# Kernel tuning notes

Measured on AMD Instinct MI355X. Metric: run time of the kernel, lower is better.

The kernel has to match this reference:

```python
import jax, jax.numpy as jnp
import numpy as np

B, S, J, D, H = 8, 256, 24, 128, 8
DEPTH = D // H  # 16


def _pos_encoding(seq_len, d_model):
    # matches position_encoding: angle = pos / 10000^(2*(i//2)/d_model);
    # even dims -> sin, odd dims -> cos. shape (1, seq_len, 1, d_model)
    pos = jnp.arange(seq_len, dtype=jnp.float32)[:, None]
    i = jnp.arange(d_model)
    rates = 1.0 / jnp.power(10000.0, (2 * (i // 2)).astype(jnp.float32) / d_model)
    ang = pos * rates[None, :]
    pe = jnp.where(i % 2 == 0, jnp.sin(ang), jnp.cos(ang))
    return pe[None, :, None, :]


def setup_inputs() -> dict:
    key = jax.random.key(0)
    ks = jax.random.split(key, 10)
    std = float(np.sqrt(1.0 / np.sqrt(D * D)))  # matches initialize()
    x = jax.random.normal(ks[0], (B, S, J, D), jnp.float32)
    # look-ahead mask on the (S-1, S-1) sub-block: 1 = masked (future)
    mask = jnp.triu(jnp.ones((S - 1, S - 1), jnp.float32), k=1)
    Wq = jax.random.normal(ks[1], (D, D), jnp.float32) * std
    bq = jnp.zeros((D,), jnp.float32)
    Wk = jax.random.normal(ks[2], (D, D), jnp.float32) * std
    bk = jnp.zeros((D,), jnp.float32)
    Wv = jax.random.normal(ks[3], (D, D), jnp.float32) * std
    bv = jnp.zeros((D,), jnp.float32)
    Wo = jax.random.normal(ks[4], (D, D), jnp.float32) * std
    bo = jnp.zeros((D,), jnp.float32)
    return {"x": x, "mask": mask, "Wq": Wq, "bq": bq, "Wk": Wk, "bk": bk,
            "Wv": Wv, "bv": bv, "Wo": Wo, "bo": bo}


def _split_heads(t):
    # (B, S, J, D) -> (B, J, H, S, DEPTH)
    b, s, j, d = t.shape
    t = t.transpose(0, 2, 1, 3)                 # (B, J, S, D)
    t = t.reshape(b, j, s, H, DEPTH)            # (B, J, S, H, DEPTH)
    return t.transpose(0, 1, 3, 2, 4)           # (B, J, H, S, DEPTH)


def reference(x, mask, Wq, bq, Wk, bk, Wv, bv, Wo, bo):
    b, s, j, d = x.shape
    x = x + _pos_encoding(S, D)[:, :s]          # broadcast over batch & joints
    # shared QKV projections (same math as linear applied on (J,B,S,D))
    q = _split_heads(jnp.einsum('bsjd,de->bsje', x, Wq) + bq)
    k = _split_heads(jnp.einsum('bsjd,de->bsje', x, Wk) + bk)
    v = _split_heads(jnp.einsum('bsjd,de->bsje', x, Wv) + bv)
    scores = jnp.einsum('bjhqd,bjhkd->bjhqk', q, k) / jnp.sqrt(
        jnp.asarray(DEPTH, x.dtype))            # (B, J, H, S, S)
    # custom partial-block masking: only the [1:, 1:] sub-block is masked
    scores = scores.at[:, :, :, 1:, 1:].add(mask * -1e9)
    w = jax.nn.softmax(scores, axis=-1)
    out = jnp.einsum('bjhqk,bjhkd->bjhqd', w, v)  # (B, J, H, S, DEPTH)
    out = out.transpose(0, 3, 1, 2, 4).reshape(b, s, j, d)
    out = jnp.einsum('bsjd,de->bsje', out, Wo) + bo
    return (out, mask)
```

## Files before the change

kernel.cpp:

```cpp
#include <hip/hip_runtime.h>
#include <hip/hip_bf16.h>
#include <math.h>

#define NB 8
#define NS 256
#define NJ 24
#define ND 128
#define NH 8
#define NDEP 16
#define NROW (NB * NS * NJ)

typedef unsigned short u16;
typedef unsigned int u32;
typedef float f32x4 __attribute__((ext_vector_type(4)));
typedef short bf16x8 __attribute__((ext_vector_type(8)));
typedef unsigned short us8 __attribute__((ext_vector_type(8)));
typedef unsigned short us4 __attribute__((ext_vector_type(4)));

#define MFMA16(a, b, c) __builtin_amdgcn_mfma_f32_16x16x32_bf16(a, b, c, 0, 0, 0)

#define QSCALE 0.36067376022224085f

__device__ __forceinline__ u16 f2bf(float f) {
    union { __hip_bfloat16 h; u16 u; } cv;
    cv.h = __float2bfloat16(f);
    return cv.u;
}
__device__ __forceinline__ u32 cvtpk(float lo, float hi) {
    u32 r;
    asm("v_cvt_pk_bf16_f32 %0, %1, %2" : "=v"(r) : "v"(lo), "v"(hi));
    return r;
}

__global__ __launch_bounds__(256) void prep_kernel(
        const float* __restrict__ Wq, const float* __restrict__ Wk,
        const float* __restrict__ Wv, const float* __restrict__ Wo,
        const float* __restrict__ mask,
        float* __restrict__ pe, u16* __restrict__ wt,
        float* __restrict__ mask_dst) {
    int idx = blockIdx.x * 256 + threadIdx.x;
    if (idx < 32768) {
        int s = idx >> 7, d = idx & 127;
        float r = __expf(-(float)(d & ~1) * (9.210340371976184f / 128.0f));
        float ang = (float)s * r;
        pe[idx] = (d & 1) ? cosf(ang) : sinf(ang);
    } else if (idx < 98304) {
        int e = idx - 32768;
        int w = e >> 14, rr = e & 16383;
        int n = rr >> 7, kk = rr & 127;
        const float* W = (w == 0) ? Wq : (w == 1) ? Wk : (w == 2) ? Wv : Wo;
        float val = W[kk * 128 + n];
        if (w == 0) val *= QSCALE;
        wt[e] = f2bf(val);
    } else {
        int e = idx - 98304;
        if (e < (NS - 1) * (NS - 1)) mask_dst[e] = mask[e];
    }
}

__global__ __launch_bounds__(256) void qkv_kernel(
        const float* __restrict__ x, const float* __restrict__ pe,
        const u16* __restrict__ wt,
        const float* __restrict__ bq, const float* __restrict__ bk,
        const float* __restrict__ bv,
        u16* __restrict__ qo, u16* __restrict__ ko, u16* __restrict__ vo) {
    __shared__ u16 xs[64][136];
    __shared__ u16 wsh[128][136];
    const int t = threadIdx.x;
    const int row0 = blockIdx.x * 64;

#pragma unroll
    for (int i = 0; i < 8; i++) {
        int f4 = t + i * 256;
        int r = f4 >> 5, c4 = (f4 & 31) * 4;
        int grow = row0 + r;
        int s = (grow / NJ) & (NS - 1);
        float4 xv = *(const float4*)&x[(size_t)grow * ND + c4];
        float4 pv = *(const float4*)&pe[s * ND + c4];
        us4 b4;
        b4[0] = f2bf(xv.x + pv.x); b4[1] = f2bf(xv.y + pv.y);
        b4[2] = f2bf(xv.z + pv.z); b4[3] = f2bf(xv.w + pv.w);
        *(us4*)&xs[r][c4] = b4;
    }

    const int l = t & 63, wv = t >> 6, gg = l >> 4, c = l & 15;
    const float* bm[3] = {bq, bk, bv};
    u16* om[3] = {qo, ko, vo};

#pragma unroll
    for (int w = 0; w < 3; w++) {
        __syncthreads();
#pragma unroll
        for (int i = 0; i < 8; i++) {
            int u8 = t + i * 256;
            int r = u8 >> 4, c8 = (u8 & 15) * 8;
            *(us8*)&wsh[r][c8] = *(const us8*)&wt[w * 16384 + r * 128 + c8];
        }
        __syncthreads();
        f32x4 acc[8] = {};
#pragma unroll
        for (int ks = 0; ks < 4; ks++) {
            bf16x8 af = *(const bf16x8*)&xs[wv * 16 + c][ks * 32 + gg * 8];
#pragma unroll
            for (int nf = 0; nf < 8; nf++) {
                bf16x8 bf_ = *(const bf16x8*)&wsh[nf * 16 + c][ks * 32 + gg * 8];
                acc[nf] = MFMA16(af, bf_, acc[nf]);
            }
        }
        __syncthreads();
        const float bscale = (w == 0) ? QSCALE : 1.0f;
#pragma unroll
        for (int nf = 0; nf < 8; nf++) {
            float bb = bm[w][nf * 16 + c] * bscale;
#pragma unroll
            for (int r = 0; r < 4; r++)
                wsh[wv * 16 + gg * 4 + r][nf * 16 + c] = f2bf(acc[nf][r] + bb);
        }
        __syncthreads();
#pragma unroll
        for (int i = 0; i < 4; i++) {
            int u8 = t + i * 256;
            int row = u8 >> 4, piece = u8 & 15;
            int grow = row0 + row;
            int b = grow / 6144, rem = grow % 6144;
            int s = rem / NJ, jj = rem % NJ;
            int hh = piece >> 1, half = piece & 1;
            us8 val = *(const us8*)&wsh[row][piece * 8];
            *(us8*)&om[w][(size_t)((b * NJ + jj) * NH + hh) * 4096 + s * 16 +
                          half * 8] = val;
        }
    }
}

__global__ __launch_bounds__(512) void attn_kernel(
        const u16* __restrict__ q, const u16* __restrict__ k,
        const u16* __restrict__ v, u16* __restrict__ o) {
    __shared__ u16 ksh[256][24];
    __shared__ uint4 vts4[16][32];

    const int t = threadIdx.x;
    const int bjh = blockIdx.x;
    const size_t base = (size_t)bjh * 4096;

    {
        int row = t >> 1, c8 = (t & 1) * 8;
        *(us8*)&ksh[row][c8] = *(const us8*)&k[base + row * 16 + c8];
    }
    {
        int r = t >> 1, h8 = (t & 1) * 8;
        us8 vv = *(const us8*)&v[base + r * 16 + h8];
        int slot = (r & 0xE0) | ((r & 12) << 1) | ((r & 16) >> 2) | (r & 3);
        int cell = slot >> 3, e = slot & 7;
#pragma unroll
        for (int dd = 0; dd < 8; dd++) {
            int d = h8 + dd;
            ((u16*)&vts4[d][cell ^ (d & 7)])[e] = vv[dd];
        }
    }
    __syncthreads();

    const int wv = t >> 6, l = t & 63, gg = l >> 4, c = l & 15;
    const int h = bjh & 7, j = (bjh >> 3) % NJ, b = bjh / (NJ * NH);
    const size_t obase = (size_t)b * 786432 + (size_t)j * 128 + h * 16 + c;
    const unsigned long long TBL = 0xBA79685F4E3D2C10ull;

#pragma unroll
    for (int slot = 0; slot < 2; slot++) {
        const int g = (int)((TBL >> ((wv * 2 + slot) * 4)) & 15);
        const int dchk = g >> 2;
        const int nch = (g == 0) ? 4 : dchk + 1;
        const int qrow = 16 * g + c;
        const int thr = (qrow == 0) ? 0x7fffffff : qrow;

        bf16x8 bq_ = {};
        if (gg < 2)
            bq_ = *(const bf16x8*)&q[base + (size_t)qrow * 16 + gg * 8];

        f32x4 oa = {};
        float ls = 0.0f;
#pragma unroll
        for (int ch = 0; ch < 4; ch++) {
            if (ch >= nch) continue;
            const bool diag = (g == 0) || (ch == dchk);
            f32x4 st[4];
            __builtin_amdgcn_s_setprio(1);
#pragma unroll
            for (int kf = 0; kf < 4; kf++) {
                bf16x8 ak = {};
                if (gg < 2)
                    ak = *(const bf16x8*)&ksh[ch * 64 + kf * 16 + c][gg * 8];
                f32x4 zz = {};
                st[kf] = MFMA16(ak, bq_, zz);
            }
            __builtin_amdgcn_s_setprio(0);
            u32 pw[8];
            if (diag) {
#pragma unroll
                for (int kf = 0; kf < 4; kf++) {
#pragma unroll
                    for (int r = 0; r < 4; r++) {
                        int key = ch * 64 + kf * 16 + gg * 4 + r;
                        float vv = (key > thr) ? -1.0e9f : st[kf][r];
                        float p = __builtin_amdgcn_exp2f(vv);
                        st[kf][r] = p;
                        ls += p;
                    }
                    pw[kf * 2]     = cvtpk(st[kf][0], st[kf][1]);
                    pw[kf * 2 + 1] = cvtpk(st[kf][2], st[kf][3]);
                }
            } else {
#pragma unroll
                for (int kf = 0; kf < 4; kf++) {
#pragma unroll
                    for (int r = 0; r < 4; r++) {
                        float p = __builtin_amdgcn_exp2f(st[kf][r]);
                        st[kf][r] = p;
                        ls += p;
                    }
                    pw[kf * 2]     = cvtpk(st[kf][0], st[kf][1]);
                    pw[kf * 2 + 1] = cvtpk(st[kf][2], st[kf][3]);
                }
            }
            uint4 a0 = make_uint4(pw[0], pw[1], pw[2], pw[3]);
            uint4 a1 = make_uint4(pw[4], pw[5], pw[6], pw[7]);
            __builtin_amdgcn_s_setprio(1);
#pragma unroll
            for (int ks = 0; ks < 2; ks++) {
                bf16x8 ap = __builtin_bit_cast(bf16x8, ks ? a1 : a0);
                uint4 vb4 = vts4[c][(ch * 8 + ks * 4 + gg) ^ (c & 7)];
                bf16x8 bv_ = __builtin_bit_cast(bf16x8, vb4);
                oa = MFMA16(ap, bv_, oa);
            }
            __builtin_amdgcn_s_setprio(0);
        }
        ls += __shfl_xor(ls, 16);
        ls += __shfl_xor(ls, 32);
        const float inv = 1.0f / ls;
#pragma unroll
        for (int r = 0; r < 4; r++) {
            float ir = __shfl(inv, gg * 4 + r);
            int s = 16 * g + gg * 4 + r;
            o[obase + (size_t)s * 3072] = f2bf(oa[r] * ir);
        }
    }
}

__global__ __launch_bounds__(256) void proj_kernel(
        const u16* __restrict__ in, const u16* __restrict__ wt,
        const float* __restrict__ bias, float* __restrict__ out) {
    __shared__ u16 xs[64][136];
    __shared__ u16 wsh[128][136];
    const int t = threadIdx.x;
    const int row0 = blockIdx.x * 64;
#pragma unroll
    for (int i = 0; i < 4; i++) {
        int u8 = t + i * 256;
        int r = u8 >> 4, c8 = (u8 & 15) * 8;
        *(us8*)&xs[r][c8] = *(const us8*)&in[(size_t)(row0 + r) * ND + c8];
    }
#pragma unroll
    for (int i = 0; i < 8; i++) {
        int u8 = t + i * 256;
        int r = u8 >> 4, c8 = (u8 & 15) * 8;
        *(us8*)&wsh[r][c8] = *(const us8*)&wt[r * 128 + c8];
    }
    __syncthreads();
    const int l = t & 63, wv = t >> 6, gg = l >> 4, c = l & 15;
    f32x4 acc[8] = {};
#pragma unroll
    for (int ks = 0; ks < 4; ks++) {
        bf16x8 af = *(const bf16x8*)&xs[wv * 16 + c][ks * 32 + gg * 8];
#pragma unroll
        for (int nf = 0; nf < 8; nf++) {
            bf16x8 bf_ = *(const bf16x8*)&wsh[nf * 16 + c][ks * 32 + gg * 8];
            acc[nf] = MFMA16(af, bf_, acc[nf]);
        }
    }
    __syncthreads();
    float* bounce = (float*)&wsh[0][0];
#pragma unroll
    for (int nf = 0; nf < 8; nf++) {
        float bb = bias[nf * 16 + c];
#pragma unroll
        for (int r = 0; r < 4; r++)
            bounce[(wv * 16 + gg * 4 + r) * 132 + nf * 16 + c] = acc[nf][r] + bb;
    }
    __syncthreads();
#pragma unroll
    for (int i = 0; i < 8; i++) {
        int idx = t + i * 256;
        int row = idx >> 5, p4 = idx & 31;
        float4 vv = *(const float4*)&bounce[row * 132 + p4 * 4];
        *(float4*)&out[(size_t)(row0 + row) * 128 + p4 * 4] = vv;
    }
}

extern "C" void kernel_launch(void* const* d_in, const int* in_sizes, int n_in,
                              void* d_out, int out_size, void* d_ws, size_t ws_size,
                              hipStream_t stream) {
    const float* x    = (const float*)d_in[0];
    const float* mask = (const float*)d_in[1];
    const float* Wq   = (const float*)d_in[2];
    const float* bq   = (const float*)d_in[3];
    const float* Wk   = (const float*)d_in[4];
    const float* bk   = (const float*)d_in[5];
    const float* Wv   = (const float*)d_in[6];
    const float* bv   = (const float*)d_in[7];
    const float* Wo   = (const float*)d_in[8];
    const float* bo   = (const float*)d_in[9];
    float* out = (float*)d_out;

    char* ws = (char*)d_ws;
    float* pe = (float*)ws;
    u16* wt  = (u16*)(ws + 131072);
    u16* qb  = (u16*)(ws + 262144);
    u16* kb  = qb + (size_t)NROW * ND;
    u16* vb  = kb + (size_t)NROW * ND;
    u16* ab  = vb + (size_t)NROW * ND;

    prep_kernel<<<639, 256, 0, stream>>>(Wq, Wk, Wv, Wo, mask, pe, wt,
                                         out + (size_t)NROW * ND);
    qkv_kernel<<<NROW / 64, 256, 0, stream>>>(x, pe, wt, bq, bk, bv, qb, kb, vb);
    attn_kernel<<<NB * NJ * NH, 512, 0, stream>>>(qb, kb, vb, ab);
    proj_kernel<<<NROW / 64, 256, 0, stream>>>(ab, wt + 3 * 16384, bo, out);
}
```

Before: 57.53 us.

## Read weight fragments directly from global and coalesce attention output writes

The QKV and output-projection kernels stop staging the 128x128 bf16 weight tile in shared memory and load MFMA B fragments straight from global (cache-resident) memory, which shrinks LDS use and removes barriers. The attention kernel now writes its output in the contiguous per-head layout (base + s*16 + c) instead of strided 2-byte scatters, and the projection kernel gathers rows from that head-major layout when loading its A tile. Together these aim to fix uncoalesced stores and to raise occupancy, at the cost of repeated global/L2 weight reads per wave and a gather on the projection input.

```diff
diff --git a/kernel.cpp b/kernel.cpp
--- a/kernel.cpp
+++ b/kernel.cpp
@@ -65,7 +65,7 @@
         const float* __restrict__ bv,
         u16* __restrict__ qo, u16* __restrict__ ko, u16* __restrict__ vo) {
     __shared__ u16 xs[64][136];
-    __shared__ u16 wsh[128][136];
+    __shared__ u16 bounce[64][136];
     const int t = threadIdx.x;
     const int row0 = blockIdx.x * 64;
 
@@ -82,6 +82,7 @@
         b4[2] = f2bf(xv.z + pv.z); b4[3] = f2bf(xv.w + pv.w);
         *(us4*)&xs[r][c4] = b4;
     }
+    __syncthreads();
 
     const int l = t & 63, wv = t >> 6, gg = l >> 4, c = l & 15;
     const float* bm[3] = {bq, bk, bv};
@@ -89,32 +90,25 @@
 
 #pragma unroll
     for (int w = 0; w < 3; w++) {
-        __syncthreads();
-#pragma unroll
-        for (int i = 0; i < 8; i++) {
-            int u8 = t + i * 256;
-            int r = u8 >> 4, c8 = (u8 & 15) * 8;
-            *(us8*)&wsh[r][c8] = *(const us8*)&wt[w * 16384 + r * 128 + c8];
-        }
-        __syncthreads();
         f32x4 acc[8] = {};
 #pragma unroll
         for (int ks = 0; ks < 4; ks++) {
             bf16x8 af = *(const bf16x8*)&xs[wv * 16 + c][ks * 32 + gg * 8];
 #pragma unroll
             for (int nf = 0; nf < 8; nf++) {
-                bf16x8 bf_ = *(const bf16x8*)&wsh[nf * 16 + c][ks * 32 + gg * 8];
+                bf16x8 bf_ = *(const bf16x8*)&wt[w * 16384 + (nf * 16 + c) * 128 +
+                                                 ks * 32 + gg * 8];
                 acc[nf] = MFMA16(af, bf_, acc[nf]);
             }
         }
-        __syncthreads();
+        if (w > 0) __syncthreads();
         const float bscale = (w == 0) ? QSCALE : 1.0f;
 #pragma unroll
         for (int nf = 0; nf < 8; nf++) {
             float bb = bm[w][nf * 16 + c] * bscale;
 #pragma unroll
             for (int r = 0; r < 4; r++)
-                wsh[wv * 16 + gg * 4 + r][nf * 16 + c] = f2bf(acc[nf][r] + bb);
+                bounce[wv * 16 + gg * 4 + r][nf * 16 + c] = f2bf(acc[nf][r] + bb);
         }
         __syncthreads();
 #pragma unroll
@@ -125,7 +119,7 @@
             int b = grow / 6144, rem = grow % 6144;
             int s = rem / NJ, jj = rem % NJ;
             int hh = piece >> 1, half = piece & 1;
-            us8 val = *(const us8*)&wsh[row][piece * 8];
+            us8 val = *(const us8*)&bounce[row][piece * 8];
             *(us8*)&om[w][(size_t)((b * NJ + jj) * NH + hh) * 4096 + s * 16 +
                           half * 8] = val;
         }
@@ -160,8 +154,6 @@
     __syncthreads();
 
     const int wv = t >> 6, l = t & 63, gg = l >> 4, c = l & 15;
-    const int h = bjh & 7, j = (bjh >> 3) % NJ, b = bjh / (NJ * NH);
-    const size_t obase = (size_t)b * 786432 + (size_t)j * 128 + h * 16 + c;
     const unsigned long long TBL = 0xBA79685F4E3D2C10ull;
 
 #pragma unroll
@@ -240,7 +232,7 @@
         for (int r = 0; r < 4; r++) {
             float ir = __shfl(inv, gg * 4 + r);
             int s = 16 * g + gg * 4 + r;
-            o[obase + (size_t)s * 3072] = f2bf(oa[r] * ir);
+            o[base + (size_t)s * 16 + c] = f2bf(oa[r] * ir);
         }
     }
 }
@@ -249,20 +241,20 @@
         const u16* __restrict__ in, const u16* __restrict__ wt,
         const float* __restrict__ bias, float* __restrict__ out) {
     __shared__ u16 xs[64][136];
-    __shared__ u16 wsh[128][136];
+    __shared__ float bounce[64][132];
     const int t = threadIdx.x;
     const int row0 = blockIdx.x * 64;
 #pragma unroll
     for (int i = 0; i < 4; i++) {
         int u8 = t + i * 256;
-        int r = u8 >> 4, c8 = (u8 & 15) * 8;
-        *(us8*)&xs[r][c8] = *(const us8*)&in[(size_t)(row0 + r) * ND + c8];
-    }
-#pragma unroll
-    for (int i = 0; i < 8; i++) {
-        int u8 = t + i * 256;
-        int r = u8 >> 4, c8 = (u8 & 15) * 8;
-        *(us8*)&wsh[r][c8] = *(const us8*)&wt[r * 128 + c8];
+        int row = u8 >> 4, piece = u8 & 15;
+        int grow = row0 + row;
+        int b = grow / 6144, rem = grow % 6144;
+        int s = rem / NJ, jj = rem % NJ;
+        int hh = piece >> 1, half = piece & 1;
+        *(us8*)&xs[row][piece * 8] =
+            *(const us8*)&in[(size_t)((b * NJ + jj) * NH + hh) * 4096 + s * 16 +
+                             half * 8];
     }
     __syncthreads();
     const int l = t & 63, wv = t >> 6, gg = l >> 4, c = l & 15;
@@ -272,25 +264,25 @@
         bf16x8 af = *(const bf16x8*)&xs[wv * 16 + c][ks * 32 + gg * 8];
 #pragma unroll
         for (int nf = 0; nf < 8; nf++) {
-            bf16x8 bf_ = *(const bf16x8*)&wsh[nf * 16 + c][ks * 32 + gg * 8];
+            bf16x8 bf_ = *(const bf16x8*)&wt[(nf * 16 + c) * 128 + ks * 32 +
+                                             gg * 8];
             acc[nf] = MFMA16(af, bf_, acc[nf]);
         }
     }
     __syncthreads();
-    float* bounce = (float*)&wsh[0][0];
 #pragma unroll
     for (int nf = 0; nf < 8; nf++) {
         float bb = bias[nf * 16 + c];
 #pragma unroll
         for (int r = 0; r < 4; r++)
-            bounce[(wv * 16 + gg * 4 + r) * 132 + nf * 16 + c] = acc[nf][r] + bb;
+            bounce[wv * 16 + gg * 4 + r][nf * 16 + c] = acc[nf][r] + bb;
     }
     __syncthreads();
 #pragma unroll
     for (int i = 0; i < 8; i++) {
         int idx = t + i * 256;
         int row = idx >> 5, p4 = idx & 31;
-        float4 vv = *(const float4*)&bounce[row * 132 + p4 * 4];
+        float4 vv = *(const float4*)&bounce[row][p4 * 4];
         *(float4*)&out[(size_t)(row0 + row) * 128 + p4 * 4] = vv;
     }
 }
```

After: 94.53 us. 64.3% more time.
